# Kernel tuning notes

Hardware: AMD Instinct MI355X
Metric: run time of the kernel (lower is better)

## Reference

```python
import jax, jax.numpy as jnp
import numpy as np

N = 50000
E = 800000
IN_F, HID, OUT_F = 512, 256, 64
KEEP = 0.5  # Dropout(0.5)


def setup_inputs() -> dict:
    key = jax.random.key(0)
    ks = jax.random.split(key, 7)
    X = jax.random.normal(ks[0], (N, IN_F), dtype=jnp.float32)
    # Xavier-uniform-style init for the two layer weights
    lim1 = float(np.sqrt(6.0 / (IN_F + HID)))
    lim2 = float(np.sqrt(6.0 / (HID + OUT_F)))
    W1 = jax.random.uniform(ks[1], (IN_F, HID), jnp.float32, -lim1, lim1)
    W2 = jax.random.uniform(ks[2], (HID, OUT_F), jnp.float32, -lim2, lim2)
    a_row = jnp.sort(jax.random.randint(ks[3], (E,), 0, N)).astype(jnp.int64)
    a_col = jax.random.randint(ks[4], (E,), 0, N).astype(jnp.int64)
    a_val = jax.random.uniform(ks[5], (E,), jnp.float32)
    drop_mask = jax.random.randint(ks[6], (N, HID), 0, 2).astype(jnp.int32)
    return {"X": X, "W1": W1, "W2": W2, "a_row": a_row, "a_col": a_col,
            "a_val": a_val, "drop_mask": drop_mask}


def _spmm(a_row, a_col, a_val, dense):
    # A @ dense where A is [N, N] sparse in COO form: gather + weighted segment-sum
    msgs = a_val[:, None] * dense[a_col]          # [E, d]
    return jax.ops.segment_sum(msgs, a_row, num_segments=N)


def reference(X, W1, W2, a_row, a_col, a_val, drop_mask):
    # layer 1: feature transform + neighbor aggregation
    h = _spmm(a_row, a_col, a_val, X @ W1)        # [N, HID]
    h = jax.nn.relu(h)
    h = h * drop_mask.astype(h.dtype) * (1.0 / KEEP)  # Dropout(0.5), train mode
    # layer 2
    out = _spmm(a_row, a_col, a_val, h @ W2)      # [N, OUT_F]
    return jax.nn.log_softmax(out, axis=1)
```

## Files before the change

kernel.cpp:

```cpp
#include <hip/hip_runtime.h>
#include <hip/hip_bf16.h>
#include <math.h>

#define NN   50000
#define EE   800000
#define INF  512
#define HIDF 256
#define OUTF 64
#define MTILES (NN/16)

using short8 = __attribute__((ext_vector_type(8))) short;
using short4v = __attribute__((ext_vector_type(4))) short;
using f32x4  = __attribute__((ext_vector_type(4))) float;
using i32x4  = __attribute__((ext_vector_type(4))) int;

typedef __attribute__((address_space(1))) const void gas_void;
typedef __attribute__((address_space(3))) void las_void;

static __device__ __forceinline__ short f2bf(float f){
  unsigned u = __builtin_bit_cast(unsigned, f);
  u += 0x7fff + ((u >> 16) & 1);
  return (short)(u >> 16);
}
static __device__ __forceinline__ float bf2f(short s){
  unsigned u = ((unsigned)(unsigned short)s) << 16;
  return __builtin_bit_cast(float, u);
}

__global__ void k_prep(const int* __restrict__ a_row, int* __restrict__ row_ptr,
                       const float* __restrict__ W1, short* __restrict__ W1p,
                       const float* __restrict__ W2, short* __restrict__ W2bT,
                       const int* __restrict__ drop, unsigned short* __restrict__ dropP){
  int b = blockIdx.x, tid = threadIdx.x;
  if (b < 196){
    int i = b * 256 + tid;
    if (i > NN) return;
    int lo = 0, hi = EE;
    while (lo < hi){ int mid = (lo + hi) >> 1; if (a_row[mid] < i) lo = mid + 1; else hi = mid; }
    row_ptr[i] = lo;
  } else if (b < 708){
    int idx = (b - 196) * 256 + tid;
    int k = idx >> 8, col = idx & 255;
    int kk = k >> 5, k2 = k & 31;
    W1p[((kk << 8) + col) * 32 + k2] = f2bf(W1[idx]);
  } else if (b < 772){
    int idx = (b - 708) * 256 + tid;
    int k = idx >> 6, n = idx & 63;
    W2bT[n * HIDF + k] = f2bf(W2[idx]);
  } else {
    int w = (b - 772) * 256 + tid;
    const i32x4* dp = (const i32x4*)(drop + w * 16);
    i32x4 m0 = __builtin_nontemporal_load(dp);
    i32x4 m1 = __builtin_nontemporal_load(dp + 1);
    i32x4 m2 = __builtin_nontemporal_load(dp + 2);
    i32x4 m3 = __builtin_nontemporal_load(dp + 3);
    unsigned bits =
        (unsigned)(m0[0] & 1)        | ((unsigned)(m0[1] & 1) << 1)  |
        ((unsigned)(m0[2] & 1) << 2) | ((unsigned)(m0[3] & 1) << 3)  |
        ((unsigned)(m1[0] & 1) << 4) | ((unsigned)(m1[1] & 1) << 5)  |
        ((unsigned)(m1[2] & 1) << 6) | ((unsigned)(m1[3] & 1) << 7)  |
        ((unsigned)(m2[0] & 1) << 8) | ((unsigned)(m2[1] & 1) << 9)  |
        ((unsigned)(m2[2] & 1) << 10)| ((unsigned)(m2[3] & 1) << 11) |
        ((unsigned)(m3[0] & 1) << 12)| ((unsigned)(m3[1] & 1) << 13) |
        ((unsigned)(m3[2] & 1) << 14)| ((unsigned)(m3[3] & 1) << 15);
    dropP[w] = (unsigned short)bits;
  }
}

__global__ __launch_bounds__(256) void k_gemm1(const float* __restrict__ X,
                                               const short* __restrict__ W1p,
                                               short* __restrict__ XW1b){
  __shared__ short lds[3][256 * 32];
  int wave = threadIdx.x >> 6, lane = threadIdx.x & 63;
  int l16 = lane & 15, quad = lane >> 4;
  int m0 = blockIdx.x * 64 + wave * 16;
  int r = min(m0 + l16, NN - 1);
  const f32x4* ap = (const f32x4*)(X + (size_t)r * INF + quad * 8);

  f32x4 acc[16];
  #pragma unroll
  for (int t = 0; t < 16; t++) acc[t] = (f32x4){0.f,0.f,0.f,0.f};

  auto stage = [&](int buf, int panel){
    const char* src = (const char*)(W1p + panel * (256 * 32));
    char* dst = (char*)&lds[buf][0];
    #pragma unroll
    for (int j = 0; j < 4; j++){
      int off = wave * 4096 + j * 1024;
      __builtin_amdgcn_global_load_lds((gas_void*)(src + off + lane * 16),
                                       (las_void*)(dst + off), 16, 0, 0);
    }
  };

  f32x4 a0[2], a1[2];
  stage(0, 0);
  a0[0] = __builtin_nontemporal_load(ap + 0);
  a1[0] = __builtin_nontemporal_load(ap + 1);
  stage(1, 1);
  a0[1] = __builtin_nontemporal_load(ap + 8);
  a1[1] = __builtin_nontemporal_load(ap + 9);

  #pragma unroll
  for (int k = 0; k < 16; k++){
    asm volatile("s_waitcnt vmcnt(6)");
    __builtin_amdgcn_sched_barrier(0);
    __builtin_amdgcn_s_barrier();
    __builtin_amdgcn_sched_barrier(0);
    f32x4 ca0 = a0[k & 1], ca1 = a1[k & 1];
    short8 af;
    af[0]=f2bf(ca0[0]); af[1]=f2bf(ca0[1]); af[2]=f2bf(ca0[2]); af[3]=f2bf(ca0[3]);
    af[4]=f2bf(ca1[0]); af[5]=f2bf(ca1[1]); af[6]=f2bf(ca1[2]); af[7]=f2bf(ca1[3]);
    int p = (k + 2 < 16) ? (k + 2) : 15;
    stage((k + 2) % 3, p);
    a0[k & 1] = __builtin_nontemporal_load(ap + p * 8);
    a1[k & 1] = __builtin_nontemporal_load(ap + p * 8 + 1);
    const short* bp = &lds[k % 3][0] + l16 * 32 + quad * 8;
    #pragma unroll
    for (int nt = 0; nt < 16; nt++){
      short8 bf = *(const short8*)(bp + nt * 512);
      acc[nt] = __builtin_amdgcn_mfma_f32_16x16x32_bf16(af, bf, acc[nt], 0, 0, 0);
    }
  }

  #pragma unroll
  for (int nt = 0; nt < 16; nt++){
    int col = nt*16 + l16;
    #pragma unroll
    for (int rr = 0; rr < 4; rr++){
      int row = m0 + quad*4 + rr;
      if (row < NN) XW1b[(size_t)row * HIDF + col] = f2bf(acc[nt][rr]);
    }
  }
}

__global__ __launch_bounds__(256) void k_spmm1(const int* __restrict__ row_ptr,
                                               const int* __restrict__ a_col,
                                               const float* __restrict__ a_val,
                                               const short* __restrict__ XW1b,
                                               const unsigned short* __restrict__ dropP,
                                               short* __restrict__ hb){
  int wave = threadIdx.x >> 6, lane = threadIdx.x & 63;
  int r = blockIdx.x * 4 + wave;
  int s = row_ptr[r], e = row_ptr[r+1];
  int g = lane >> 4;
  int c16 = lane & 15;
  int d = e - s;

  int   lim = d < 64 ? d : 64;
  bool  lv  = lane < lim;
  float myv = lv ? a_val[s + lane] : 0.f;
  int   myc = lv ? a_col[s + lane] : 0;

  float acc[16];
  #pragma unroll
  for (int j = 0; j < 16; j++) acc[j] = 0.f;

  int nsteps = (lim + 3) >> 2;
  for (int t = 0; t < nsteps; t += 2){
    int e0 = 4*t + g, e1 = 4*t + 4 + g;
    float v0 = __shfl(myv, e0);  int c0 = __shfl(myc, e0);
    float v1 = __shfl(myv, e1);  int c1 = __shfl(myc, e1);
    const short* p0 = XW1b + (c0 << 8) + c16 * 16;
    const short* p1 = XW1b + (c1 << 8) + c16 * 16;
    short8 xa0 = *(const short8*)(p0), xb0 = *(const short8*)(p0 + 8);
    short8 xa1 = *(const short8*)(p1), xb1 = *(const short8*)(p1 + 8);
    #pragma unroll
    for (int j = 0; j < 8; j++){
      acc[j]   += v0 * bf2f(xa0[j]);  acc[j+8] += v0 * bf2f(xb0[j]);
      acc[j]   += v1 * bf2f(xa1[j]);  acc[j+8] += v1 * bf2f(xb1[j]);
    }
  }
  if (d > 64){
    for (int i = s + 64 + g; i < e; i += 4){
      float v = a_val[i];  int c = a_col[i];
      const short* p = XW1b + (c << 8) + c16 * 16;
      short8 xa = *(const short8*)(p), xb = *(const short8*)(p + 8);
      #pragma unroll
      for (int j = 0; j < 8; j++){
        acc[j] += v * bf2f(xa[j]);  acc[j+8] += v * bf2f(xb[j]);
      }
    }
  }

  #pragma unroll
  for (int j = 0; j < 16; j++){
    acc[j] += __shfl_xor(acc[j], 16);
    acc[j] += __shfl_xor(acc[j], 32);
  }
  if (lane < 16){
    unsigned bits = dropP[r * 16 + c16];
    short8 o0, o1;
    #pragma unroll
    for (int j = 0; j < 8; j++){
      o0[j] = f2bf(fmaxf(acc[j],   0.f) * (((bits >> j)     & 1) ? 2.0f : 0.0f));
      o1[j] = f2bf(fmaxf(acc[j+8], 0.f) * (((bits >> (j+8)) & 1) ? 2.0f : 0.0f));
    }
    short* hp = hb + (size_t)r * HIDF + c16 * 16;
    *(short8*)(hp)     = o0;
    *(short8*)(hp + 8) = o1;
  }
}

__global__ __launch_bounds__(256) void k_gemm2(const short* __restrict__ A,
                                               const short* __restrict__ BT,
                                               short* __restrict__ C){
  int wave = threadIdx.x >> 6, lane = threadIdx.x & 63;
  int tile_m = blockIdx.x * 4 + wave;
  if (tile_m >= MTILES) return;
  int m0 = tile_m * 16, l16 = lane & 15, quad = lane >> 4;

  f32x4 acc[4];
  #pragma unroll
  for (int t = 0; t < 4; t++) acc[t] = (f32x4){0.f,0.f,0.f,0.f};

  const short* ar = A + (size_t)(m0 + l16) * HIDF + quad * 8;
  for (int kk = 0; kk < HIDF/32; kk++){
    short8 af = *(const short8*)(ar + kk * 32);
    #pragma unroll
    for (int nt = 0; nt < 4; nt++){
      short8 bf = *(const short8*)(BT + (size_t)(nt*16 + l16) * HIDF + kk*32 + quad*8);
      acc[nt] = __builtin_amdgcn_mfma_f32_16x16x32_bf16(af, bf, acc[nt], 0, 0, 0);
    }
  }
  #pragma unroll
  for (int nt = 0; nt < 4; nt++){
    int col = nt*16 + l16;
    #pragma unroll
    for (int r = 0; r < 4; r++)
      C[(size_t)(m0 + quad*4 + r) * OUTF + col] = f2bf(acc[nt][r]);
  }
}

__global__ __launch_bounds__(256) void k_spmm2_lsm(const int* __restrict__ row_ptr,
                                                   const int* __restrict__ a_col,
                                                   const float* __restrict__ a_val,
                                                   const short* __restrict__ HW2b,
                                                   float* __restrict__ out){
  int wave = threadIdx.x >> 6, lane = threadIdx.x & 63;
  int r = blockIdx.x * 4 + wave;
  int s = row_ptr[r], e = row_ptr[r+1];
  int g8 = lane >> 3;
  int c8 = lane & 7;
  int d = e - s;

  int   lim = d < 64 ? d : 64;
  bool  lv  = lane < lim;
  float myv = lv ? a_val[s + lane] : 0.f;
  int   myc = lv ? a_col[s + lane] : 0;

  float acc[8];
  #pragma unroll
  for (int j = 0; j < 8; j++) acc[j] = 0.f;

  int nsteps = (lim + 7) >> 3;
  for (int t = 0; t < nsteps; t += 2){
    int e0 = 8*t + g8, e1 = 8*t + 8 + g8;
    float v0 = __shfl(myv, e0);  int c0 = __shfl(myc, e0);
    float v1 = __shfl(myv, e1);  int c1 = __shfl(myc, e1);
    short8 x0 = *(const short8*)(HW2b + (c0 << 6) + c8 * 8);
    short8 x1 = *(const short8*)(HW2b + (c1 << 6) + c8 * 8);
    #pragma unroll
    for (int j = 0; j < 8; j++){
      acc[j] += v0 * bf2f(x0[j]);
      acc[j] += v1 * bf2f(x1[j]);
    }
  }
  if (d > 64){
    for (int i = s + 64 + g8; i < e; i += 8){
      float v = a_val[i];  int c = a_col[i];
      short8 x = *(const short8*)(HW2b + (c << 6) + c8 * 8);
      #pragma unroll
      for (int j = 0; j < 8; j++) acc[j] += v * bf2f(x[j]);
    }
  }

  #pragma unroll
  for (int j = 0; j < 8; j++){
    acc[j] += __shfl_xor(acc[j], 8);
    acc[j] += __shfl_xor(acc[j], 16);
    acc[j] += __shfl_xor(acc[j], 32);
  }
  float m = acc[0];
  #pragma unroll
  for (int j = 1; j < 8; j++) m = fmaxf(m, acc[j]);
  #pragma unroll
  for (int o = 1; o <= 4; o <<= 1) m = fmaxf(m, __shfl_xor(m, o));
  float ssum = 0.f;
  #pragma unroll
  for (int j = 0; j < 8; j++) ssum += expf(acc[j] - m);
  #pragma unroll
  for (int o = 1; o <= 4; o <<= 1) ssum += __shfl_xor(ssum, o);
  float ls = logf(ssum);
  if (lane < 8){
    f32x4 o0 = { acc[0]-m-ls, acc[1]-m-ls, acc[2]-m-ls, acc[3]-m-ls };
    f32x4 o1 = { acc[4]-m-ls, acc[5]-m-ls, acc[6]-m-ls, acc[7]-m-ls };
    float* op = out + (size_t)r * OUTF + c8 * 8;
    *(f32x4*)(op)     = o0;
    *(f32x4*)(op + 4) = o1;
  }
}

extern "C" void kernel_launch(void* const* d_in, const int* in_sizes, int n_in,
                              void* d_out, int out_size, void* d_ws, size_t ws_size,
                              hipStream_t stream) {
  const float* X      = (const float*)d_in[0];
  const float* W1     = (const float*)d_in[1];
  const float* W2     = (const float*)d_in[2];
  const int*   a_row  = (const int*)d_in[3];
  const int*   a_col  = (const int*)d_in[4];
  const float* a_val  = (const float*)d_in[5];
  const int*   drop   = (const int*)d_in[6];
  float*       out    = (float*)d_out;

  char* ws = (char*)d_ws;
  int*            row_ptr = (int*)           (ws);
  short*          W1p     = (short*)         (ws + 200704);
  short*          W2bT    = (short*)         (ws + 462848);
  short*          XW1b    = (short*)         (ws + 495616);
  short*          hb      = (short*)         (ws + 26095616);
  short*          HW2b    = (short*)         (ws + 51695616);
  unsigned short* dropP   = (unsigned short*)(ws + 58095616);

  k_prep<<<3897, 256, 0, stream>>>(a_row, row_ptr, W1, W1p, W2, W2bT, drop, dropP);
  k_gemm1<<<(NN + 63)/64, 256, 0, stream>>>(X, W1p, XW1b);
  k_spmm1<<<NN/4, 256, 0, stream>>>(row_ptr, a_col, a_val, XW1b, dropP, hb);
  k_gemm2<<<(MTILES + 3)/4, 256, 0, stream>>>(hb, W2bT, HW2b);
  k_spmm2_lsm<<<NN/4, 256, 0, stream>>>(row_ptr, a_col, a_val, HW2b, out);
}
```

Before: 327.8 us.

## Fuse layer-1 SpMM epilogue with the H@W2 GEMM through shared memory

The first sparse aggregation kernel now processes 16 rows per 1024-thread block and writes the ReLU/dropout result into an LDS tile instead of global memory. Four of its waves then run the 16x64 MFMA product against W2 directly, so the separate GEMM2 launch and the 25 MB bf16 hidden-activation round trip through HBM are gone. The cost is a block-wide barrier after the irregular gather, where waves with short rows wait on the longest row, and 12 of 16 waves sit idle during the GEMM. The 1024-thread launch bound may also limit occupancy.

```diff
diff --git a/kernel.cpp b/kernel.cpp
--- a/kernel.cpp
+++ b/kernel.cpp
@@ -133,14 +133,16 @@
   }
 }
 
-__global__ __launch_bounds__(256) void k_spmm1(const int* __restrict__ row_ptr,
-                                               const int* __restrict__ a_col,
-                                               const float* __restrict__ a_val,
-                                               const short* __restrict__ XW1b,
-                                               const unsigned short* __restrict__ dropP,
-                                               short* __restrict__ hb){
+__global__ __launch_bounds__(1024, 1) void k_spmm1f(const int* __restrict__ row_ptr,
+                                                    const int* __restrict__ a_col,
+                                                    const float* __restrict__ a_val,
+                                                    const short* __restrict__ XW1b,
+                                                    const unsigned short* __restrict__ dropP,
+                                                    const short* __restrict__ W2bT,
+                                                    short* __restrict__ HW2b){
+  __shared__ short h_tile[16][264];
   int wave = threadIdx.x >> 6, lane = threadIdx.x & 63;
-  int r = blockIdx.x * 4 + wave;
+  int r = blockIdx.x * 16 + wave;
   int s = row_ptr[r], e = row_ptr[r+1];
   int g = lane >> 4;
   int c16 = lane & 15;
@@ -195,39 +197,24 @@
       o0[j] = f2bf(fmaxf(acc[j],   0.f) * (((bits >> j)     & 1) ? 2.0f : 0.0f));
       o1[j] = f2bf(fmaxf(acc[j+8], 0.f) * (((bits >> (j+8)) & 1) ? 2.0f : 0.0f));
     }
-    short* hp = hb + (size_t)r * HIDF + c16 * 16;
-    *(short8*)(hp)     = o0;
-    *(short8*)(hp + 8) = o1;
-  }
-}
-
-__global__ __launch_bounds__(256) void k_gemm2(const short* __restrict__ A,
-                                               const short* __restrict__ BT,
-                                               short* __restrict__ C){
-  int wave = threadIdx.x >> 6, lane = threadIdx.x & 63;
-  int tile_m = blockIdx.x * 4 + wave;
-  if (tile_m >= MTILES) return;
-  int m0 = tile_m * 16, l16 = lane & 15, quad = lane >> 4;
-
-  f32x4 acc[4];
-  #pragma unroll
-  for (int t = 0; t < 4; t++) acc[t] = (f32x4){0.f,0.f,0.f,0.f};
-
-  const short* ar = A + (size_t)(m0 + l16) * HIDF + quad * 8;
-  for (int kk = 0; kk < HIDF/32; kk++){
-    short8 af = *(const short8*)(ar + kk * 32);
-    #pragma unroll
-    for (int nt = 0; nt < 4; nt++){
-      short8 bf = *(const short8*)(BT + (size_t)(nt*16 + l16) * HIDF + kk*32 + quad*8);
-      acc[nt] = __builtin_amdgcn_mfma_f32_16x16x32_bf16(af, bf, acc[nt], 0, 0, 0);
-    }
-  }
-  #pragma unroll
-  for (int nt = 0; nt < 4; nt++){
-    int col = nt*16 + l16;
-    #pragma unroll
-    for (int r = 0; r < 4; r++)
-      C[(size_t)(m0 + quad*4 + r) * OUTF + col] = f2bf(acc[nt][r]);
+    *(short8*)(&h_tile[wave][c16 * 16])     = o0;
+    *(short8*)(&h_tile[wave][c16 * 16 + 8]) = o1;
+  }
+  __syncthreads();
+
+  if (wave < 4){
+    int l16 = lane & 15, quad = lane >> 4;
+    f32x4 c4 = (f32x4){0.f,0.f,0.f,0.f};
+    #pragma unroll
+    for (int kk = 0; kk < HIDF/32; kk++){
+      short8 af = *(const short8*)(&h_tile[l16][kk*32 + quad*8]);
+      short8 bf = *(const short8*)(W2bT + (size_t)(wave*16 + l16) * HIDF + kk*32 + quad*8);
+      c4 = __builtin_amdgcn_mfma_f32_16x16x32_bf16(af, bf, c4, 0, 0, 0);
+    }
+    int base = blockIdx.x * 16;
+    #pragma unroll
+    for (int rr = 0; rr < 4; rr++)
+      HW2b[(size_t)(base + quad*4 + rr) * OUTF + wave*16 + l16] = f2bf(c4[rr]);
   }
 }
 
@@ -317,13 +304,11 @@
   short*          W1p     = (short*)         (ws + 200704);
   short*          W2bT    = (short*)         (ws + 462848);
   short*          XW1b    = (short*)         (ws + 495616);
-  short*          hb      = (short*)         (ws + 26095616);
-  short*          HW2b    = (short*)         (ws + 51695616);
-  unsigned short* dropP   = (unsigned short*)(ws + 58095616);
+  short*          HW2b    = (short*)         (ws + 26095616);
+  unsigned short* dropP   = (unsigned short*)(ws + 32495616);
 
   k_prep<<<3897, 256, 0, stream>>>(a_row, row_ptr, W1, W1p, W2, W2bT, drop, dropP);
   k_gemm1<<<(NN + 63)/64, 256, 0, stream>>>(X, W1p, XW1b);
-  k_spmm1<<<NN/4, 256, 0, stream>>>(row_ptr, a_col, a_val, XW1b, dropP, hb);
-  k_gemm2<<<(MTILES + 3)/4, 256, 0, stream>>>(hb, W2bT, HW2b);
+  k_spmm1f<<<NN/16, 1024, 0, stream>>>(row_ptr, a_col, a_val, XW1b, dropP, W2bT, HW2b);
   k_spmm2_lsm<<<NN/4, 256, 0, stream>>>(row_ptr, a_col, a_val, HW2b, out);
 }
```

Result: no change. 327.9 us (+0.0%).
